# Performance work log

Measured on AMD Instinct MI355X. Metric: run time of the kernel, lower is better.

## Reference

```python
import jax, jax.numpy as jnp
import numpy as np

B, T, N_EMBD = 4, 2048, 1024
N_EXP, TOP_K = 8, 2
EPS = 1e-9
EVAL_CAPACITY_FACTOR = 2.0
MIN_CAPACITY = 4
# eval-mode capacity: min(group_size, int(group_size * cap_factor / n_exp)), floored at min_capacity
CAPACITY = max(min(T, int(T * EVAL_CAPACITY_FACTOR / N_EXP)), MIN_CAPACITY)  # 512
THRESHOLD = np.array([EPS, 0.2], dtype=np.float32)  # threshold_eval buffer: [eps, *thresholds]


def setup_inputs() -> dict:
    key = jax.random.key(0)
    k1, k2, k3 = jax.random.split(key, 3)
    x = jax.random.normal(k1, (B, T, N_EMBD), dtype=jnp.float32)
    w_g = jax.random.normal(k2, (N_EXP, N_EMBD), dtype=jnp.float32) * 0.02
    probs = jax.random.uniform(k3, (TOP_K, B, T), dtype=jnp.float32)
    return {"x": x, "w_g": w_g, "probs": probs}


def reference(x, w_g, probs):
    # gate logits and softmax gates
    gate_logits = jnp.einsum('btd,ed->bte', x, w_g)          # [B,T,E]
    raw_gates = jax.nn.softmax(gate_logits, axis=-1)
    top_v, top_i = jax.lax.top_k(raw_gates, TOP_K)           # [B,T,k]
    gates = jnp.transpose(top_v, (2, 0, 1))                  # [k,B,T]
    gate_idx = jnp.transpose(top_i, (2, 0, 1))               # [k,B,T]
    one_hot_gate = jax.nn.one_hot(gate_idx, N_EXP, dtype=jnp.float32)  # [k,B,T,E]

    # renormalize top-k gates
    denom = jnp.clip(jnp.sum(gates, axis=0, keepdims=True), EPS, None)
    gates = gates / denom

    # stochastic thresholding (top-1 always routes)
    thr = jnp.asarray(THRESHOLD)[:, None, None]              # [k,1,1]
    should_route = probs < gates / jnp.clip(thr, EPS, None)
    should_route = should_route.at[0].set(True)
    mask = one_hot_gate * should_route[..., None].astype(jnp.float32)  # [k,B,T,E]

    # exclusive cumsum over tokens (dim T)
    mask_cumsum = jnp.cumsum(mask, axis=-2) - mask           # [k,B,T,E]

    masks, positions = [], []
    prev = jnp.zeros((B, 1, N_EXP), dtype=jnp.float32)
    cap_f = float(CAPACITY)
    for n in range(TOP_K):  # small fixed loop over routing ranks
        pos = (mask_cumsum[n] + prev) * mask[n]              # [B,T,E]
        m_n = mask[n] * (pos < cap_f).astype(jnp.float32)    # capacity drop
        prev = jnp.sum(m_n, axis=1, keepdims=True) + prev
        masks.append(m_n)
        positions.append(jnp.sum(pos, axis=-1))              # [B,T]
    mask = jnp.stack(masks)                                  # [k,B,T,E]
    positions = jnp.stack(positions)                         # [k,B,T]

    mask_flat = jnp.sum(mask, axis=-1)                       # [k,B,T] in {0,1}
    gates = gates * mask_flat

    # position one-hot; out-of-range positions map to all-zero rows (== safe_one_hot + slice)
    pos_oh = jax.nn.one_hot(positions.astype(jnp.int32), CAPACITY, dtype=jnp.float32)  # [k,B,T,C]

    # combine tensor: sum over k of gates * mask_flat * one_hot(expert) x one_hot(position)
    combine = jnp.einsum('kbt,kbte,kbtc->btec', gates * mask_flat, one_hot_gate, pos_oh)  # [B,T,E,C]

    dispatch_hard = (combine > 0).astype(combine.dtype)
    # straight-through dispatch tensor
    dispatch = dispatch_hard + combine - jax.lax.stop_gradient(combine)
    return dispatch, combine
```

## Files before the change

kernel.cpp:

```cpp
#include <hip/hip_runtime.h>

#define BB 4
#define TT 2048
#define DD 1024
#define EE 8
#define CAP 512
#define NTOK (BB*TT)
#define OUT_HALF ((size_t)NTOK * EE * CAP)

__global__ __launch_bounds__(256) void gate_kernel(
    const float* __restrict__ x, const float* __restrict__ w,
    const float* __restrict__ probs,
    int* __restrict__ e0, int* __restrict__ e1enc,
    float* __restrict__ v0, float* __restrict__ v1)
{
    const int wave = threadIdx.x >> 6;
    const int lane = threadIdx.x & 63;
    const int token = blockIdx.x * 4 + wave;
    const float4* xt4 = (const float4*)(x + (size_t)token * DD);
    const float4* w4  = (const float4*)w;

    float acc[EE];
    #pragma unroll
    for (int e = 0; e < EE; ++e) acc[e] = 0.f;

    #pragma unroll
    for (int i = 0; i < 4; ++i) {
        float4 xv = xt4[i * 64 + lane];
        #pragma unroll
        for (int e = 0; e < EE; ++e) {
            float4 wv = w4[e * 256 + i * 64 + lane];
            acc[e] = fmaf(xv.x, wv.x, acc[e]);
            acc[e] = fmaf(xv.y, wv.y, acc[e]);
            acc[e] = fmaf(xv.z, wv.z, acc[e]);
            acc[e] = fmaf(xv.w, wv.w, acc[e]);
        }
    }
    #pragma unroll
    for (int e = 0; e < EE; ++e) {
        #pragma unroll
        for (int off = 32; off > 0; off >>= 1)
            acc[e] += __shfl_xor(acc[e], off, 64);
    }

    if (lane == 0) {
        float mx = acc[0];
        #pragma unroll
        for (int e = 1; e < EE; ++e) mx = fmaxf(mx, acc[e]);
        float ex[EE]; float Z = 0.f;
        #pragma unroll
        for (int e = 0; e < EE; ++e) { ex[e] = expf(acc[e] - mx); Z += ex[e]; }
        int i0 = 0;
        #pragma unroll
        for (int e = 1; e < EE; ++e) if (ex[e] > ex[i0]) i0 = e;
        int i1 = (i0 == 0) ? 1 : 0;
        #pragma unroll
        for (int e = 0; e < EE; ++e) if (e != i0 && ex[e] > ex[i1]) i1 = e;
        float t0 = ex[i0] / Z, t1 = ex[i1] / Z;
        float den = fmaxf(t0 + t1, 1e-9f);
        float g0 = t0 / den, g1 = t1 / den;
        float p1 = probs[NTOK + token];
        int route = (p1 < g1 / 0.2f) ? 1 : 0;
        e0[token] = i0;
        e1enc[token] = i1 | (route << 3);
        v0[token] = g0; v1[token] = g1;
    }
}

__global__ __launch_bounds__(64) void scan_kernel(
    const int* __restrict__ e0, const int* __restrict__ e1enc,
    int* __restrict__ t0, int* __restrict__ t1)
{
    const int b = blockIdx.x >> 3;
    const int e = blockIdx.x & 7;
    const int lane = threadIdx.x;
    const unsigned long long lt = (lane == 63) ? 0x7fffffffffffffffull
                                               : ((1ull << lane) - 1ull);
    const int base_tok = b * TT;

    int ev[32];
    #pragma unroll
    for (int c = 0; c < 32; ++c) ev[c] = e0[base_tok + c * 64 + lane];

    int cnt = 0;
    #pragma unroll
    for (int c = 0; c < 32; ++c) {
        bool hit = (ev[c] == e);
        unsigned long long m = __ballot(hit);
        if (hit) {
            int pos = cnt + __popcll(m & lt);
            t0[base_tok + c * 64 + lane] = (pos < CAP) ? e * CAP + pos : -1;
        }
        cnt += __popcll(m);
    }

    int e1v[32];
    #pragma unroll
    for (int c = 0; c < 32; ++c) e1v[c] = e1enc[base_tok + c * 64 + lane];

    int cnt1 = min(cnt, CAP);
    #pragma unroll
    for (int c = 0; c < 32; ++c) {
        bool sel = ((e1v[c] & 7) == e);
        bool hit = sel && (e1v[c] & 8);
        unsigned long long m = __ballot(hit);
        if (sel) {
            int pos = cnt1 + __popcll(m & lt);
            t1[base_tok + c * 64 + lane] = (hit && pos < CAP) ? e * CAP + pos : -1;
        }
        cnt1 += __popcll(m);
    }
}

__global__ __launch_bounds__(256) void fill_scatter_kernel(
    const int* __restrict__ t0, const int* __restrict__ t1,
    const float* __restrict__ v0, const float* __restrict__ v1,
    float4* __restrict__ out)
{
    const int token = blockIdx.x;
    const int tid = threadIdx.x;
    const int a0 = t0[token];
    const int a1 = t1[token];
    const float g0 = v0[token];
    const float g1 = v1[token];

    float4* drow = out + (size_t)token * 1024;
    float4* crow = out + (OUT_HALF / 4) + (size_t)token * 1024;

    #pragma unroll
    for (int i = 0; i < 4; ++i) {
        const int f = i * 1024 + tid * 4;
        float4 d, c;
        d.x = (f + 0 == a0 || f + 0 == a1) ? 1.f : 0.f;
        d.y = (f + 1 == a0 || f + 1 == a1) ? 1.f : 0.f;
        d.z = (f + 2 == a0 || f + 2 == a1) ? 1.f : 0.f;
        d.w = (f + 3 == a0 || f + 3 == a1) ? 1.f : 0.f;
        c.x = (f + 0 == a0) ? g0 : ((f + 0 == a1) ? g1 : 0.f);
        c.y = (f + 1 == a0) ? g0 : ((f + 1 == a1) ? g1 : 0.f);
        c.z = (f + 2 == a0) ? g0 : ((f + 2 == a1) ? g1 : 0.f);
        c.w = (f + 3 == a0) ? g0 : ((f + 3 == a1) ? g1 : 0.f);
        drow[i * 256 + tid] = d;
        crow[i * 256 + tid] = c;
    }
}

extern "C" void kernel_launch(void* const* d_in, const int* in_sizes, int n_in,
                              void* d_out, int out_size, void* d_ws, size_t ws_size,
                              hipStream_t stream) {
    const float* x     = (const float*)d_in[0];
    const float* w     = (const float*)d_in[1];
    const float* probs = (const float*)d_in[2];
    float* out = (float*)d_out;

    int*   e0 = (int*)d_ws;
    int*   e1 = e0 + NTOK;
    int*   t0 = e1 + NTOK;
    int*   t1 = t0 + NTOK;
    float* v0 = (float*)(t1 + NTOK);
    float* v1 = v0 + NTOK;

    gate_kernel<<<2048, 256, 0, stream>>>(x, w, probs, e0, e1, v0, v1);
    scan_kernel<<<32, 64, 0, stream>>>(e0, e1, t0, t1);
    fill_scatter_kernel<<<8192, 256, 0, stream>>>(t0, t1, v0, v1, (float4*)out);
}
```

Measured before the change: 68.41 us.

## Replace dense fill kernel with bulk zeroing plus sparse scatter from scan

The per-token fill kernel computed every dispatch and combine element with comparisons. It is replaced by a pure zero-store kernel over the whole output, followed by a scan kernel that writes only the nonzero dispatch and combine entries directly. The intermediate slot arrays t0 and t1 are dropped from the workspace. The output is still written in full once. The gain depends on whether plain zero stores beat compare-and-store, since the tiny 32-block scatter adds its own latency after the zero pass.

```diff
diff --git a/kernel.cpp b/kernel.cpp
--- a/kernel.cpp
+++ b/kernel.cpp
@@ -7,6 +7,8 @@
 #define CAP 512
 #define NTOK (BB*TT)
 #define OUT_HALF ((size_t)NTOK * EE * CAP)
+
+typedef float f32x4 __attribute__((ext_vector_type(4)));
 
 __global__ __launch_bounds__(256) void gate_kernel(
     const float* __restrict__ x, const float* __restrict__ w,
@@ -67,9 +69,20 @@
     }
 }
 
-__global__ __launch_bounds__(64) void scan_kernel(
+__global__ __launch_bounds__(256) void zero_kernel(f32x4* __restrict__ out)
+{
+    const size_t stride = (size_t)4096 * 256;
+    size_t idx = (size_t)blockIdx.x * 256 + threadIdx.x;
+    f32x4 z = (f32x4)(0.f);
+    #pragma unroll
+    for (int k = 0; k < 16; ++k)
+        out[idx + (size_t)k * stride] = z;
+}
+
+__global__ __launch_bounds__(64) void scan_scatter_kernel(
     const int* __restrict__ e0, const int* __restrict__ e1enc,
-    int* __restrict__ t0, int* __restrict__ t1)
+    const float* __restrict__ v0, const float* __restrict__ v1,
+    float* __restrict__ dispatch, float* __restrict__ combine)
 {
     const int b = blockIdx.x >> 3;
     const int e = blockIdx.x & 7;
@@ -89,7 +102,12 @@
         unsigned long long m = __ballot(hit);
         if (hit) {
             int pos = cnt + __popcll(m & lt);
-            t0[base_tok + c * 64 + lane] = (pos < CAP) ? e * CAP + pos : -1;
+            if (pos < CAP) {
+                int tok = base_tok + c * 64 + lane;
+                size_t oi = ((size_t)tok * EE + e) * CAP + pos;
+                dispatch[oi] = 1.0f;
+                combine[oi]  = v0[tok];
+            }
         }
         cnt += __popcll(m);
     }
@@ -101,46 +119,18 @@
     int cnt1 = min(cnt, CAP);
     #pragma unroll
     for (int c = 0; c < 32; ++c) {
-        bool sel = ((e1v[c] & 7) == e);
-        bool hit = sel && (e1v[c] & 8);
+        bool hit = ((e1v[c] & 7) == e) && (e1v[c] & 8);
         unsigned long long m = __ballot(hit);
-        if (sel) {
+        if (hit) {
             int pos = cnt1 + __popcll(m & lt);
-            t1[base_tok + c * 64 + lane] = (hit && pos < CAP) ? e * CAP + pos : -1;
+            if (pos < CAP) {
+                int tok = base_tok + c * 64 + lane;
+                size_t oi = ((size_t)tok * EE + e) * CAP + pos;
+                dispatch[oi] = 1.0f;
+                combine[oi]  = v1[tok];
+            }
         }
         cnt1 += __popcll(m);
-    }
-}
-
-__global__ __launch_bounds__(256) void fill_scatter_kernel(
-    const int* __restrict__ t0, const int* __restrict__ t1,
-    const float* __restrict__ v0, const float* __restrict__ v1,
-    float4* __restrict__ out)
-{
-    const int token = blockIdx.x;
-    const int tid = threadIdx.x;
-    const int a0 = t0[token];
-    const int a1 = t1[token];
-    const float g0 = v0[token];
-    const float g1 = v1[token];
-
-    float4* drow = out + (size_t)token * 1024;
-    float4* crow = out + (OUT_HALF / 4) + (size_t)token * 1024;
-
-    #pragma unroll
-    for (int i = 0; i < 4; ++i) {
-        const int f = i * 1024 + tid * 4;
-        float4 d, c;
-        d.x = (f + 0 == a0 || f + 0 == a1) ? 1.f : 0.f;
-        d.y = (f + 1 == a0 || f + 1 == a1) ? 1.f : 0.f;
-        d.z = (f + 2 == a0 || f + 2 == a1) ? 1.f : 0.f;
-        d.w = (f + 3 == a0 || f + 3 == a1) ? 1.f : 0.f;
-        c.x = (f + 0 == a0) ? g0 : ((f + 0 == a1) ? g1 : 0.f);
-        c.y = (f + 1 == a0) ? g0 : ((f + 1 == a1) ? g1 : 0.f);
-        c.z = (f + 2 == a0) ? g0 : ((f + 2 == a1) ? g1 : 0.f);
-        c.w = (f + 3 == a0) ? g0 : ((f + 3 == a1) ? g1 : 0.f);
-        drow[i * 256 + tid] = d;
-        crow[i * 256 + tid] = c;
     }
 }
 
@@ -154,12 +144,11 @@
 
     int*   e0 = (int*)d_ws;
     int*   e1 = e0 + NTOK;
-    int*   t0 = e1 + NTOK;
-    int*   t1 = t0 + NTOK;
-    float* v0 = (float*)(t1 + NTOK);
+    float* v0 = (float*)(e1 + NTOK);
     float* v1 = v0 + NTOK;
 
     gate_kernel<<<2048, 256, 0, stream>>>(x, w, probs, e0, e1, v0, v1);
-    scan_kernel<<<32, 64, 0, stream>>>(e0, e1, t0, t1);
-    fill_scatter_kernel<<<8192, 256, 0, stream>>>(t0, t1, v0, v1, (float4*)out);
+    zero_kernel<<<4096, 256, 0, stream>>>((f32x4*)out);
+    scan_scatter_kernel<<<32, 64, 0, stream>>>(e0, e1, v0, v1,
+                                               out, out + OUT_HALF);
 }
```

After: 94.55 us. 38.2% more time.
